# Kernel optimization log

Hardware: AMD Instinct MI355X
Metric: run time of the kernel (lower is better)

Reference implementation:

```python
import jax, jax.numpy as jnp
import numpy as np

N, E, G, H = 50000, 400000, 64, 128
NODE_IN, EDGE_IN = 3, 3
LN_EPS = 1e-5


def _ln(x, g, b):
    mu = jnp.mean(x, axis=-1, keepdims=True)
    var = jnp.mean((x - mu) ** 2, axis=-1, keepdims=True)
    return (x - mu) / jnp.sqrt(var + LN_EPS) * g + b


def _enc(x, w1, b1, w2, b2, w3, b3, g, bb):
    # Linear->ReLU->Linear->ReLU->Linear->LayerNorm (dropout = identity at eval)
    h = jax.nn.relu(x @ w1 + b1)
    h = jax.nn.relu(h @ w2 + b2)
    return _ln(h @ w3 + b3, g, bb)


def _gcn(x, w, b, src, dst, n):
    xw = x @ w
    deg = jax.ops.segment_sum(jnp.ones(src.shape[0], x.dtype), dst, num_segments=n) + 1.0
    dinv = jax.lax.rsqrt(deg)
    msgs = xw[src] * (dinv[src] * dinv[dst])[:, None]
    agg = jax.ops.segment_sum(msgs, dst, num_segments=n) + xw * (dinv * dinv)[:, None]
    return agg + b


def setup_inputs() -> dict:
    keys = iter(jax.random.split(jax.random.key(0), 64))

    def nrm(shape, s=0.05):
        return jax.random.normal(next(keys), shape, jnp.float32) * s

    inp = {
        "x": jax.random.normal(next(keys), (N, NODE_IN), jnp.float32),
        "edge_index": jax.random.randint(next(keys), (2, E), 0, N),
        "edge_attr": jax.random.normal(next(keys), (E, EDGE_IN), jnp.float32),
        "batch": jnp.sort(jax.random.randint(next(keys), (N,), 0, G)),
    }

    def lin(prefix, din, dout):
        inp[prefix + "_w"] = nrm((din, dout))
        inp[prefix + "_b"] = jnp.zeros((dout,), jnp.float32)

    for p, din in (("ne", NODE_IN), ("ee", EDGE_IN)):
        lin(p + "1", din, H); lin(p + "2", H, H); lin(p + "3", H, H)
        inp[p + "_g"] = jnp.ones((H,), jnp.float32)
        inp[p + "_bb"] = jnp.zeros((H,), jnp.float32)
    lin("g1", H, H); lin("g2", H, H)
    lin("gp1", H, H); lin("gp2", H, H)
    inp["gp_g"] = jnp.ones((H,), jnp.float32)
    inp["gp_bb"] = jnp.zeros((H,), jnp.float32)
    lin("ep1", 4 * H, 2 * H); lin("ep2", 2 * H, H)
    lin("ep3", H, H // 2); lin("ep4", H // 2, 1)
    return inp


def reference(x, edge_index, edge_attr, batch,
              ne1_w, ne1_b, ne2_w, ne2_b, ne3_w, ne3_b, ne_g, ne_bb,
              ee1_w, ee1_b, ee2_w, ee2_b, ee3_w, ee3_b, ee_g, ee_bb,
              g1_w, g1_b, g2_w, g2_b,
              gp1_w, gp1_b, gp2_w, gp2_b, gp_g, gp_bb,
              ep1_w, ep1_b, ep2_w, ep2_b, ep3_w, ep3_b, ep4_w, ep4_b):
    src, dst = edge_index[0], edge_index[1]
    h = _enc(x, ne1_w, ne1_b, ne2_w, ne2_b, ne3_w, ne3_b, ne_g, ne_bb)       # [N,H]
    ef = _enc(edge_attr, ee1_w, ee1_b, ee2_w, ee2_b, ee3_w, ee3_b, ee_g, ee_bb)  # [E,H]
    h = jax.nn.relu(_gcn(h, g1_w, g1_b, src, dst, N))
    h = _gcn(h, g2_w, g2_b, src, dst, N)
    # global mean pool per graph
    sums = jax.ops.segment_sum(h, batch, num_segments=G)
    cnts = jax.ops.segment_sum(jnp.ones((N,), h.dtype), batch, num_segments=G)
    gmean = sums / jnp.maximum(cnts, 1.0)[:, None]
    gf = jax.nn.relu(gmean @ gp1_w + gp1_b)
    gf = _ln(gf @ gp2_w + gp2_b, gp_g, gp_bb)                                 # [G,H]
    # vectorized edge-score MLP (original does a per-edge Python loop)
    comb = jnp.concatenate([h[src], h[dst], gf[batch[src]], ef], axis=-1)     # [E,4H]
    e = jnp.tanh(comb @ ep1_w + ep1_b)
    e = jnp.tanh(e @ ep2_w + ep2_b)
    e = jax.nn.relu(e @ ep3_w + ep3_b)
    return jax.nn.sigmoid(e @ ep4_w + ep4_b)                                  # [E,1]
```

## Files before the change

### kernel.cpp

```cpp
#include <hip/hip_runtime.h>
#include <math.h>

#define NN 50000
#define NE 400000
#define NG 64
#define HD 128
#define LN_EPS 1e-5f

typedef unsigned short u16;
typedef unsigned int u32;
typedef __attribute__((ext_vector_type(8))) short short8;
typedef __attribute__((ext_vector_type(4))) float f32x4;

#define MFMA16(a,b,c) __builtin_amdgcn_mfma_f32_16x16x32_bf16((a),(b),(c),0,0,0)

__device__ __forceinline__ u16 f2bf(float f) {
    union { float f; u32 u; } v; v.f = f;
    u32 r = v.u + 0x7FFFu + ((v.u >> 16) & 1u);
    return (u16)(r >> 16);
}
__device__ __forceinline__ float bf2f(u32 hs) {
    union { u32 u; float f; } v; v.u = hs << 16;
    return v.f;
}
__device__ __forceinline__ float fast_rcp(float x) {
    float r; asm("v_rcp_f32 %0, %1" : "=v"(r) : "v"(x)); return r;
}
__device__ __forceinline__ float fast_exp2(float x) {
    float r; asm("v_exp_f32 %0, %1" : "=v"(r) : "v"(x)); return r;
}
__device__ __forceinline__ u32 cvtpk(float lo, float hi) {
    u32 r; asm("v_cvt_pk_bf16_f32 %0, %1, %2" : "=v"(r) : "v"(lo), "v"(hi)); return r;
}
__device__ __forceinline__ float fast_tanh(float x) {
    return fmaf(-2.f, fast_rcp(1.f + fast_exp2(2.885390082f * x)), 1.f);
}
__device__ __forceinline__ float fast_sigmoid(float x) {
    return fast_rcp(1.f + fast_exp2(-1.442695041f * x));
}

__device__ __forceinline__ int swzr(int row) {
    return (row & 7) ^ ((row & 8) >> 2);
}

__device__ __forceinline__ short8 loadA(const u16* buf, int mi, int kk, int l) {
    int row = mi*16 + (l & 15);
    int ci  = (kk*4 + (l >> 4)) ^ swzr(l & 15);
    return *(const short8*)(buf + row*128 + (ci << 3));
}
__device__ __forceinline__ short8 loadB(const u16* wp, int nt, int ks, int nk, int l) {
    return *(const short8*)(wp + (((nt*nk + ks)*64 + l) << 3));
}

__device__ __forceinline__ void storeQuad(u32* buf, int R, int c, int l,
                                          float v0, float v1, float v2, float v3)
{
    int cw = c >> 1;
    int par = l & 1;
    float send = par ? v0 : v1;
    float recv = __shfl_xor(send, 1);
    int row = R + par;
    u32 word = par ? cvtpk(recv, v1) : cvtpk(v0, recv);
    buf[row*64 + (((cw >> 2) ^ swzr(row & 15)) << 2) + (cw & 3)] = word;
    send = par ? v2 : v3;
    recv = __shfl_xor(send, 1);
    row = R + 2 + par;
    word = par ? cvtpk(recv, v3) : cvtpk(v2, recv);
    buf[row*64 + (((cw >> 2) ^ swzr(row & 15)) << 2) + (cw & 3)] = word;
}

__device__ __forceinline__ void copyChunkOut(const u32* chunk, u32* gout, int n0, int t)
{
    for (int it = 0; it < 16; ++it) {
        int dw = it*256 + t;
        int row = dw >> 6, cw = dw & 63;
        if (n0 + row < NN)
            gout[(size_t)(n0 + row)*64 + cw] =
                chunk[row*64 + (((cw >> 2) ^ swzr(row & 15)) << 2) + (cw & 3)];
    }
}

__global__ __launch_bounds__(256)
void pack_all(const float* __restrict__ ee2w, const float* __restrict__ ee3w,
              const float* __restrict__ p1w,  const float* __restrict__ p2w,
              const float* __restrict__ p3w,  const float* __restrict__ ne2w,
              const float* __restrict__ ne3w, const float* __restrict__ g1w,
              const float* __restrict__ g2w,  u16* __restrict__ wpk)
{
    int idx = blockIdx.x*256 + threadIdx.x;
    if (idx >= 270336) return;
    const float* w; int K, N, local;
    if      (idx < 16384)  { w = ee2w; K = 128; N = 128; local = idx; }
    else if (idx < 32768)  { w = ee3w; K = 128; N = 128; local = idx - 16384; }
    else if (idx < 163840) { w = p1w;  K = 512; N = 256; local = idx - 32768; }
    else if (idx < 196608) { w = p2w;  K = 256; N = 128; local = idx - 163840; }
    else if (idx < 204800) { w = p3w;  K = 128; N = 64;  local = idx - 196608; }
    else if (idx < 221184) { w = ne2w; K = 128; N = 128; local = idx - 204800; }
    else if (idx < 237568) { w = ne3w; K = 128; N = 128; local = idx - 221184; }
    else if (idx < 253952) { w = g1w;  K = 128; N = 128; local = idx - 237568; }
    else                   { w = g2w;  K = 128; N = 128; local = idx - 253952; }
    int e = local & 7, l = (local >> 3) & 63, r = local >> 9;
    int nk = K >> 5;
    int nt = r / nk, kk = r % nk;
    int k = kk*32 + ((l >> 4) << 3) + e;
    int n = nt*16 + (l & 15);
    wpk[idx] = f2bf(w[k*N + n]);
}

__global__ __launch_bounds__(256)
void deg_count_int(const int* __restrict__ ei, int* __restrict__ degi)
{
    int e = blockIdx.x*256 + threadIdx.x;
    if (e < NE) atomicAdd(&degi[ei[NE + e]], 1);
}

__global__ __launch_bounds__(1024)
void scan_excl(const int* __restrict__ cnt, int* __restrict__ rp,
               float* __restrict__ dinv)
{
    __shared__ int wsum[16];
    __shared__ int carry;
    int t = threadIdx.x, lane = t & 63, w = t >> 6;
    int base = 0;
    for (int off = 0; off < NN; off += 4096) {
        int i0 = off + t*4;
        int v0 = (i0   < NN) ? cnt[i0]   : 0;
        int v1 = (i0+1 < NN) ? cnt[i0+1] : 0;
        int v2 = (i0+2 < NN) ? cnt[i0+2] : 0;
        int v3 = (i0+3 < NN) ? cnt[i0+3] : 0;
        int tot = v0 + v1 + v2 + v3;
        int s = tot;
#pragma unroll
        for (int d = 1; d < 64; d <<= 1) { int u = __shfl_up(s, d); if (lane >= d) s += u; }
        if (lane == 63) wsum[w] = s;
        __syncthreads();
        if (w == 0) {
            int wv = (lane < 16) ? wsum[lane] : 0;
            int ss = wv;
#pragma unroll
            for (int d = 1; d < 16; d <<= 1) { int u = __shfl_up(ss, d); if (lane >= d) ss += u; }
            if (lane < 16) wsum[lane] = ss - wv;
            if (lane == 15) carry = ss;
        }
        __syncthreads();
        int excl = base + wsum[w] + s - tot;
        if (i0   < NN) { rp[i0]   = excl;              dinv[i0]   = rsqrtf((float)v0 + 1.f); }
        if (i0+1 < NN) { rp[i0+1] = excl + v0;         dinv[i0+1] = rsqrtf((float)v1 + 1.f); }
        if (i0+2 < NN) { rp[i0+2] = excl + v0 + v1;    dinv[i0+2] = rsqrtf((float)v2 + 1.f); }
        if (i0+3 < NN) { rp[i0+3] = excl + v0 + v1 + v2; dinv[i0+3] = rsqrtf((float)v3 + 1.f); }
        base += carry;
        __syncthreads();
    }
    if (t == 0) rp[NN] = base;
}

__global__ __launch_bounds__(256)
void fill_csr(const int* __restrict__ ei, const int* __restrict__ rp,
              int* __restrict__ cursor, int* __restrict__ sadj)
{
    int e = blockIdx.x*256 + threadIdx.x;
    if (e >= NE) return;
    int d = ei[NE + e];
    int slot = atomicAdd(&cursor[d], 1);
    sadj[rp[d] + slot] = ei[e];
}

__global__ __launch_bounds__(256, 4)
void enc_mfma(const float* __restrict__ x,
              const float* __restrict__ w1, const float* __restrict__ b1,
              const u16* __restrict__ w2p, const float* __restrict__ b2,
              const u16* __restrict__ w3p, const float* __restrict__ b3,
              const float* __restrict__ gg, const float* __restrict__ bb,
              const u16* __restrict__ g1p, const float* __restrict__ dinv,
              u32* __restrict__ xw1p)
{
    __shared__ u16 chunkA[64*HD];
    __shared__ u16 chunkB[64*HD];
    __shared__ float sX[192];
    __shared__ float sDi[64];
    __shared__ float rstat[128];

    const int t = threadIdx.x;
    const int l = t & 63;
    const int wid = t >> 6;
    const int n0 = blockIdx.x * 64;

    if (t < 192) sX[t] = (n0*3 + t < NN*3) ? x[n0*3 + t] : 0.f;
    if (t < 64)  sDi[t] = (n0 + t < NN) ? dinv[n0 + t] : 0.f;
    __syncthreads();

    for (int it = 0; it < 16; ++it) {
        int dw = it*256 + t;
        int e = dw >> 6, cd = dw & 63;
        int c0 = cd*2;
        float x0 = sX[e*3], x1 = sX[e*3+1], x2 = sX[e*3+2];
        float v0 = b1[c0]   + x0*w1[c0]   + x1*w1[HD+c0]   + x2*w1[2*HD+c0];
        float v1 = b1[c0+1] + x0*w1[c0+1] + x1*w1[HD+c0+1] + x2*w1[2*HD+c0+1];
        v0 = fmaxf(v0, 0.f); v1 = fmaxf(v1, 0.f);
        int ci = cd >> 2;
        ((u32*)chunkA)[e*64 + ((ci ^ swzr(e & 15)) << 2) + (cd & 3)] = cvtpk(v0, v1);
    }
    __syncthreads();

    {
        f32x4 acc[4][2];
#pragma unroll
        for (int ni = 0; ni < 2; ++ni) {
            float b = b2[(2*wid + ni)*16 + (l & 15)];
#pragma unroll
            for (int mi = 0; mi < 4; ++mi) acc[mi][ni] = (f32x4){b,b,b,b};
        }
#pragma unroll
        for (int kk = 0; kk < 4; ++kk) {
            short8 af[4];
#pragma unroll
            for (int mi = 0; mi < 4; ++mi) af[mi] = loadA(chunkA, mi, kk, l);
#pragma unroll
            for (int ni = 0; ni < 2; ++ni) {
                short8 bw = loadB(w2p, 2*wid + ni, kk, 4, l);
#pragma unroll
                for (int mi = 0; mi < 4; ++mi) acc[mi][ni] = MFMA16(af[mi], bw, acc[mi][ni]);
            }
        }
#pragma unroll
        for (int ni = 0; ni < 2; ++ni) {
            int col = (2*wid + ni)*16 + (l & 15);
#pragma unroll
            for (int mi = 0; mi < 4; ++mi) {
                int R = mi*16 + ((l >> 4) << 2);
                storeQuad((u32*)chunkB, R, col, l,
                          fmaxf(acc[mi][ni][0], 0.f), fmaxf(acc[mi][ni][1], 0.f),
                          fmaxf(acc[mi][ni][2], 0.f), fmaxf(acc[mi][ni][3], 0.f));
            }
        }
    }
    __syncthreads();

    {
        f32x4 acc[4][2];
#pragma unroll
        for (int ni = 0; ni < 2; ++ni) {
            float b = b3[(2*wid + ni)*16 + (l & 15)];
#pragma unroll
            for (int mi = 0; mi < 4; ++mi) acc[mi][ni] = (f32x4){b,b,b,b};
        }
#pragma unroll
        for (int kk = 0; kk < 4; ++kk) {
            short8 af[4];
#pragma unroll
            for (int mi = 0; mi < 4; ++mi) af[mi] = loadA(chunkB, mi, kk, l);
#pragma unroll
            for (int ni = 0; ni < 2; ++ni) {
                short8 bw = loadB(w3p, 2*wid + ni, kk, 4, l);
#pragma unroll
                for (int mi = 0; mi < 4; ++mi) acc[mi][ni] = MFMA16(af[mi], bw, acc[mi][ni]);
            }
        }
#pragma unroll
        for (int ni = 0; ni < 2; ++ni) {
            int col = (2*wid + ni)*16 + (l & 15);
#pragma unroll
            for (int mi = 0; mi < 4; ++mi) {
                int R = mi*16 + ((l >> 4) << 2);
                storeQuad((u32*)chunkA, R, col, l,
                          acc[mi][ni][0], acc[mi][ni][1], acc[mi][ni][2], acc[mi][ni][3]);
            }
        }
    }
    __syncthreads();

    {
        int e = wid*16 + (l >> 2);
        int q = l & 3;
        const u32* rowp = (const u32*)chunkA + e*64;
        float s = 0.f, sq = 0.f;
#pragma unroll
        for (int i = 0; i < 16; ++i) {
            u32 pk = rowp[q*16 + ((i + e) & 15)];
            float a = bf2f(pk & 0xffffu), b = bf2f(pk >> 16);
            s += a + b;
            sq = fmaf(a, a, fmaf(b, b, sq));
        }
        s  += __shfl_xor(s, 1);  sq += __shfl_xor(sq, 1);
        s  += __shfl_xor(s, 2);  sq += __shfl_xor(sq, 2);
        if (q == 0) {
            float mu = s * (1.f/HD);
            rstat[e] = mu;
            rstat[64 + e] = rsqrtf(sq*(1.f/HD) - mu*mu + LN_EPS);
        }
    }
    __syncthreads();

    for (int it = 0; it < 16; ++it) {
        int pd = it*256 + t;
        int row = pd >> 6, cwd = pd & 63;
        int ci = (cwd >> 2) ^ swzr(row & 15);
        int col = ci*8 + (cwd & 3)*2;
        u32 pk = ((u32*)chunkA)[pd];
        float mu = rstat[row], ri = rstat[64 + row];
        float v0 = (bf2f(pk & 0xffffu) - mu)*ri*gg[col]     + bb[col];
        float v1 = (bf2f(pk >> 16)     - mu)*ri*gg[col + 1] + bb[col + 1];
        ((u32*)chunkA)[pd] = cvtpk(v0, v1);
    }
    __syncthreads();

    {
        f32x4 acc[4][2];
#pragma unroll
        for (int mi = 0; mi < 4; ++mi)
#pragma unroll
            for (int ni = 0; ni < 2; ++ni) acc[mi][ni] = (f32x4){0.f,0.f,0.f,0.f};
#pragma unroll
        for (int kk = 0; kk < 4; ++kk) {
            short8 af[4];
#pragma unroll
            for (int mi = 0; mi < 4; ++mi) af[mi] = loadA(chunkA, mi, kk, l);
#pragma unroll
            for (int ni = 0; ni < 2; ++ni) {
                short8 bw = loadB(g1p, 2*wid + ni, kk, 4, l);
#pragma unroll
                for (int mi = 0; mi < 4; ++mi) acc[mi][ni] = MFMA16(af[mi], bw, acc[mi][ni]);
            }
        }
#pragma unroll
        for (int ni = 0; ni < 2; ++ni) {
            int col = (2*wid + ni)*16 + (l & 15);
#pragma unroll
            for (int mi = 0; mi < 4; ++mi) {
                int R = mi*16 + ((l >> 4) << 2);
                storeQuad((u32*)chunkB, R, col, l,
                          acc[mi][ni][0]*sDi[R], acc[mi][ni][1]*sDi[R+1],
                          acc[mi][ni][2]*sDi[R+2], acc[mi][ni][3]*sDi[R+3]);
            }
        }
    }
    __syncthreads();
    copyChunkOut((const u32*)chunkB, xw1p, n0, t);
}

__global__ __launch_bounds__(256, 4)
void gcn_agg1_mfma(const u16* __restrict__ xw1p, const int* __restrict__ rp,
                   const int* __restrict__ sadj, const float* __restrict__ dinv,
                   const float* __restrict__ g1b, const u16* __restrict__ g2p,
                   u32* __restrict__ xw2p)
{
    __shared__ u16 chunkA[64*HD];
    __shared__ u16 chunkB[64*HD];
    __shared__ float sDi[64];
    __shared__ float sB[HD];

    const int t = threadIdx.x;
    const int l = t & 63;
    const int wid = t >> 6;
    const int n0 = blockIdx.x * 64;

    if (t < 64)  sDi[t] = (n0 + t < NN) ? dinv[n0 + t] : 0.f;
    if (t < HD)  sB[t] = g1b[t];
    __syncthreads();

    {
        int s = t >> 2, part = t & 3, n = n0 + s;
        float acc[32];
#pragma unroll
        for (int j = 0; j < 32; ++j) acc[j] = 0.f;
        float di = 0.f;
        if (n < NN) {
            di = sDi[s];
            const short8* selfp = (const short8*)(xw1p + (size_t)n*HD + part*32);
#pragma unroll
            for (int w = 0; w < 4; ++w) {
                short8 v = selfp[w];
#pragma unroll
                for (int j = 0; j < 8; ++j) acc[w*8+j] += bf2f((u16)v[j]);
            }
            int k1 = rp[n+1];
            for (int k = rp[n]; k < k1; ++k) {
                const short8* rp8 = (const short8*)(xw1p + (size_t)sadj[k]*HD + part*32);
#pragma unroll
                for (int w = 0; w < 4; ++w) {
                    short8 v = rp8[w];
#pragma unroll
                    for (int j = 0; j < 8; ++j) acc[w*8+j] += bf2f((u16)v[j]);
                }
            }
        }
#pragma unroll
        for (int p = 0; p < 16; ++p) {
            float v0 = fmaxf(fmaf(acc[2*p],   di, sB[part*32 + 2*p]),   0.f);
            float v1 = fmaxf(fmaf(acc[2*p+1], di, sB[part*32 + 2*p+1]), 0.f);
            int cw = part*16 + p;
            ((u32*)chunkA)[s*64 + (((cw >> 2) ^ swzr(s & 15)) << 2) + (cw & 3)] = cvtpk(v0, v1);
        }
    }
    __syncthreads();

    {
        f32x4 acc[4][2];
#pragma unroll
        for (int mi = 0; mi < 4; ++mi)
#pragma unroll
            for (int ni = 0; ni < 2; ++ni) acc[mi][ni] = (f32x4){0.f,0.f,0.f,0.f};
#pragma unroll
        for (int kk = 0; kk < 4; ++kk) {
            short8 af[4];
#pragma unroll
            for (int mi = 0; mi < 4; ++mi) af[mi] = loadA(chunkA, mi, kk, l);
#pragma unroll
            for (int ni = 0; ni < 2; ++ni) {
                short8 bw = loadB(g2p, 2*wid + ni, kk, 4, l);
#pragma unroll
                for (int mi = 0; mi < 4; ++mi) acc[mi][ni] = MFMA16(af[mi], bw, acc[mi][ni]);
            }
        }
#pragma unroll
        for (int ni = 0; ni < 2; ++ni) {
            int col = (2*wid + ni)*16 + (l & 15);
#pragma unroll
            for (int mi = 0; mi < 4; ++mi) {
                int R = mi*16 + ((l >> 4) << 2);
                storeQuad((u32*)chunkB, R, col, l,
                          acc[mi][ni][0]*sDi[R], acc[mi][ni][1]*sDi[R+1],
                          acc[mi][ni][2]*sDi[R+2], acc[mi][ni][3]*sDi[R+3]);
            }
        }
    }
    __syncthreads();
    copyChunkOut((const u32*)chunkB, xw2p, n0, t);
}

__global__ __launch_bounds__(256)
void gcn_agg2_gather(const u16* __restrict__ xw2p, const int* __restrict__ rp,
                     const int* __restrict__ sadj, const float* __restrict__ dinv,
                     const float* __restrict__ g2b, u32* __restrict__ hbw)
{
    int t = threadIdx.x;
    int s = t >> 2, part = t & 3;
    int n = blockIdx.x * 64 + s;
    if (n >= NN) return;
    float acc[32];
#pragma unroll
    for (int j = 0; j < 32; ++j) acc[j] = 0.f;
    const short8* selfp = (const short8*)(xw2p + (size_t)n*HD + part*32);
#pragma unroll
    for (int w = 0; w < 4; ++w) {
        short8 v = selfp[w];
#pragma unroll
        for (int j = 0; j < 8; ++j) acc[w*8+j] += bf2f((u16)v[j]);
    }
    int k1 = rp[n+1];
    for (int k = rp[n]; k < k1; ++k) {
        const short8* rp8 = (const short8*)(xw2p + (size_t)sadj[k]*HD + part*32);
#pragma unroll
        for (int w = 0; w < 4; ++w) {
            short8 v = rp8[w];
#pragma unroll
            for (int j = 0; j < 8; ++j) acc[w*8+j] += bf2f((u16)v[j]);
        }
    }
    float di = dinv[n];
    u32* hb = hbw + (size_t)n*64 + part*16;
#pragma unroll
    for (int p = 0; p < 16; ++p) {
        float v0 = fmaf(acc[2*p],   di, g2b[part*32 + 2*p]);
        float v1 = fmaf(acc[2*p+1], di, g2b[part*32 + 2*p+1]);
        hb[p] = cvtpk(v0, v1);
    }
}

#define POOL_B 512
__global__ __launch_bounds__(128)
void pool_sorted(const u16* __restrict__ h, const int* __restrict__ batch,
                 float* __restrict__ sums, float* __restrict__ cnts)
{
    int b = blockIdx.x, j = threadIdx.x;
    int n0 = (int)(((long long)NN * b) / POOL_B);
    int n1 = (int)(((long long)NN * (b+1)) / POOL_B);
    int g = -1; float acc = 0.f, cl = 0.f;
    for (int n = n0; n < n1; ++n) {
        int bg = batch[n];
        if (bg != g) {
            if (g >= 0) {
                atomicAdd(&sums[g*HD + j], acc);
                if (j == 0) atomicAdd(&cnts[g], cl);
            }
            g = bg; acc = 0.f; cl = 0.f;
        }
        acc += bf2f(h[(size_t)n*HD + j]);
        cl += 1.f;
    }
    if (g >= 0) {
        atomicAdd(&sums[g*HD + j], acc);
        if (j == 0) atomicAdd(&cnts[g], cl);
    }
}

__global__ __launch_bounds__(128)
void graph_feat(const float* __restrict__ sums, const float* __restrict__ cnts,
                const float* __restrict__ w1, const float* __restrict__ b1,
                const float* __restrict__ w2, const float* __restrict__ b2,
                const float* __restrict__ gg, const float* __restrict__ bb,
                u16* __restrict__ gf16)
{
    int gi = blockIdx.x, j = threadIdx.x;
    __shared__ float s0[HD];
    __shared__ float s1[HD];
    __shared__ float part[4];
    __shared__ float stat[2];
    float cnt = fmaxf(cnts[gi], 1.f);
    s0[j] = sums[gi*HD + j] / cnt;
    __syncthreads();
    float a = b1[j];
    for (int i = 0; i < HD; ++i) a = fmaf(s0[i], w1[i*HD + j], a);
    s1[j] = fmaxf(a, 0.f);
    __syncthreads();
    a = b2[j];
    for (int i = 0; i < HD; ++i) a = fmaf(s1[i], w2[i*HD + j], a);
    float s = a, q = a*a;
    for (int o = 32; o > 0; o >>= 1) { s += __shfl_down(s, o); q += __shfl_down(q, o); }
    int wid = j >> 6, lane = j & 63;
    if (lane == 0) { part[wid] = s; part[2 + wid] = q; }
    __syncthreads();
    if (j == 0) {
        float S = part[0] + part[1], Q = part[2] + part[3];
        float mu = S * (1.f/HD);
        stat[0] = mu;
        stat[1] = Q * (1.f/HD) - mu*mu;
    }
    __syncthreads();
    float v = (a - stat[0]) * rsqrtf(stat[1] + LN_EPS) * gg[j] + bb[j];
    gf16[gi*HD + j] = f2bf(v);
}

__device__ __forceinline__ void stageRows(u16* dst, const u16* __restrict__ srcBase,
                                          const int* ridx, int t)
{
    int e = t >> 2, part = t & 3;
    const u16* src = srcBase + (size_t)ridx[e]*HD + part*32;
    u16* drow = dst + e*128;
    int re = swzr(e & 15);
#pragma unroll
    for (int w = 0; w < 4; ++w) {
        int ci = (part*4 + w) ^ re;
        *(short8*)(drow + (ci << 3)) = *(const short8*)(src + w*8);
    }
}

__global__ __launch_bounds__(256, 2)
void edge_mlp_mfma(const u16* __restrict__ hbf, const u16* __restrict__ gfbf,
                   const int* __restrict__ ei, const int* __restrict__ batch,
                   const float* __restrict__ ea,
                   const float* __restrict__ ew1, const float* __restrict__ eb1,
                   const u16* __restrict__ ew2p, const float* __restrict__ eb2,
                   const u16* __restrict__ ew3p, const float* __restrict__ eb3,
                   const float* __restrict__ egm, const float* __restrict__ ebb,
                   const u16* __restrict__ p1wp, const float* __restrict__ p1b,
                   const u16* __restrict__ p2wp, const float* __restrict__ p2b,
                   const u16* __restrict__ p3wp, const float* __restrict__ p3b,
                   const float* __restrict__ p4w, const float* __restrict__ p4b,
                   float* __restrict__ out)
{
    __shared__ u16 bufChunk[64*HD];
    __shared__ u16 bufWide[64*256];
    __shared__ float sEa[192];
    __shared__ int sGf[64];
    __shared__ float rstat[128];

    const int t = threadIdx.x;
    const int l = t & 63;
    const int wid = t >> 6;
    const int e0 = blockIdx.x * 64;

    const int eRow = t >> 2, part = t & 3;
    int srcN = ei[e0 + eRow];
    int dstN = ei[NE + e0 + eRow];
    if (part == 0) sGf[eRow] = batch[srcN];
    short8 rs[4], rd[4];
    {
        const short8* ps = (const short8*)(hbf + (size_t)srcN*HD + part*32);
        const short8* pd = (const short8*)(hbf + (size_t)dstN*HD + part*32);
#pragma unroll
        for (int w = 0; w < 4; ++w) { rs[w] = ps[w]; rd[w] = pd[w]; }
    }

    if (t < 192) sEa[t] = ea[e0*3 + t];
    __syncthreads();

    for (int it = 0; it < 16; ++it) {
        int dw = it*256 + t;
        int e = dw >> 6, cd = dw & 63;
        int c0 = cd*2;
        float x0 = sEa[e*3], x1 = sEa[e*3+1], x2 = sEa[e*3+2];
        float v0 = eb1[c0]   + x0*ew1[c0]   + x1*ew1[HD+c0]   + x2*ew1[2*HD+c0];
        float v1 = eb1[c0+1] + x0*ew1[c0+1] + x1*ew1[HD+c0+1] + x2*ew1[2*HD+c0+1];
        v0 = fmaxf(v0, 0.f); v1 = fmaxf(v1, 0.f);
        int ci = cd >> 2;
        ((u32*)bufChunk)[e*64 + ((ci ^ swzr(e & 15)) << 2) + (cd & 3)] = cvtpk(v0, v1);
    }
    __syncthreads();

    {
        f32x4 acc[4][2];
#pragma unroll
        for (int ni = 0; ni < 2; ++ni) {
            float b = eb2[(2*wid + ni)*16 + (l & 15)];
#pragma unroll
            for (int mi = 0; mi < 4; ++mi) acc[mi][ni] = (f32x4){b,b,b,b};
        }
#pragma unroll
        for (int kk = 0; kk < 4; ++kk) {
            short8 af[4];
#pragma unroll
            for (int mi = 0; mi < 4; ++mi) af[mi] = loadA(bufChunk, mi, kk, l);
#pragma unroll
            for (int ni = 0; ni < 2; ++ni) {
                short8 bw = loadB(ew2p, 2*wid + ni, kk, 4, l);
#pragma unroll
                for (int mi = 0; mi < 4; ++mi) acc[mi][ni] = MFMA16(af[mi], bw, acc[mi][ni]);
            }
        }
#pragma unroll
        for (int ni = 0; ni < 2; ++ni) {
            int col = (2*wid + ni)*16 + (l & 15);
#pragma unroll
            for (int mi = 0; mi < 4; ++mi) {
                int R = mi*16 + ((l >> 4) << 2);
                storeQuad((u32*)bufWide, R, col, l,
                          fmaxf(acc[mi][ni][0], 0.f), fmaxf(acc[mi][ni][1], 0.f),
                          fmaxf(acc[mi][ni][2], 0.f), fmaxf(acc[mi][ni][3], 0.f));
            }
        }
    }
    __syncthreads();

    {
        f32x4 acc[4][2];
#pragma unroll
        for (int ni = 0; ni < 2; ++ni) {
            float b = eb3[(2*wid + ni)*16 + (l & 15)];
#pragma unroll
            for (int mi = 0; mi < 4; ++mi) acc[mi][ni] = (f32x4){b,b,b,b};
        }
#pragma unroll
        for (int kk = 0; kk < 4; ++kk) {
            short8 af[4];
#pragma unroll
            for (int mi = 0; mi < 4; ++mi) af[mi] = loadA(bufWide, mi, kk, l);
#pragma unroll
            for (int ni = 0; ni < 2; ++ni) {
                short8 bw = loadB(ew3p, 2*wid + ni, kk, 4, l);
#pragma unroll
                for (int mi = 0; mi < 4; ++mi) acc[mi][ni] = MFMA16(af[mi], bw, acc[mi][ni]);
            }
        }
#pragma unroll
        for (int ni = 0; ni < 2; ++ni) {
            int col = (2*wid + ni)*16 + (l & 15);
#pragma unroll
            for (int mi = 0; mi < 4; ++mi) {
                int R = mi*16 + ((l >> 4) << 2);
                storeQuad((u32*)bufChunk, R, col, l,
                          acc[mi][ni][0], acc[mi][ni][1], acc[mi][ni][2], acc[mi][ni][3]);
            }
        }
    }
    __syncthreads();

    {
        u16* drow0 = bufWide + eRow*128;
        u16* drow1 = bufWide + 8192 + eRow*128;
        int re = swzr(eRow & 15);
#pragma unroll
        for (int w = 0; w < 4; ++w) {
            int ci = (part*4 + w) ^ re;
            *(short8*)(drow0 + (ci << 3)) = rs[w];
            *(short8*)(drow1 + (ci << 3)) = rd[w];
        }
    }

    {
        int e = wid*16 + (l >> 2);
        int q = l & 3;
        const u32* rowp = (const u32*)bufChunk + e*64;
        float s = 0.f, sq = 0.f;
#pragma unroll
        for (int i = 0; i < 16; ++i) {
            u32 pk = rowp[q*16 + ((i + e) & 15)];
            float a = bf2f(pk & 0xffffu), b = bf2f(pk >> 16);
            s += a + b;
            sq = fmaf(a, a, fmaf(b, b, sq));
        }
        s  += __shfl_xor(s, 1);  sq += __shfl_xor(sq, 1);
        s  += __shfl_xor(s, 2);  sq += __shfl_xor(sq, 2);
        if (q == 0) {
            float mu = s * (1.f/HD);
            rstat[e] = mu;
            rstat[64 + e] = rsqrtf(sq*(1.f/HD) - mu*mu + LN_EPS);
        }
    }
    __syncthreads();

    for (int it = 0; it < 16; ++it) {
        int pd = it*256 + t;
        int row = pd >> 6, cwd = pd & 63;
        int ci = (cwd >> 2) ^ swzr(row & 15);
        int col = ci*8 + (cwd & 3)*2;
        u32 pk = ((u32*)bufChunk)[pd];
        float mu = rstat[row], ri = rstat[64 + row];
        float v0 = (bf2f(pk & 0xffffu) - mu)*ri*egm[col]     + ebb[col];
        float v1 = (bf2f(pk >> 16)     - mu)*ri*egm[col + 1] + ebb[col + 1];
        ((u32*)bufChunk)[pd] = cvtpk(v0, v1);
    }
    __syncthreads();

    f32x4 acc1[4][4];
#pragma unroll
    for (int ni = 0; ni < 4; ++ni) {
        float b = p1b[(4*wid + ni)*16 + (l & 15)];
#pragma unroll
        for (int mi = 0; mi < 4; ++mi) acc1[mi][ni] = (f32x4){b,b,b,b};
    }
#pragma unroll
    for (int kk = 0; kk < 4; ++kk) {
        short8 af[4];
#pragma unroll
        for (int mi = 0; mi < 4; ++mi) af[mi] = loadA(bufChunk, mi, kk, l);
#pragma unroll
        for (int ni = 0; ni < 4; ++ni) {
            short8 bw = loadB(p1wp, 4*wid + ni, 12 + kk, 16, l);
#pragma unroll
            for (int mi = 0; mi < 4; ++mi) acc1[mi][ni] = MFMA16(af[mi], bw, acc1[mi][ni]);
        }
    }
#pragma unroll
    for (int kk = 0; kk < 4; ++kk) {
        short8 af[4];
#pragma unroll
        for (int mi = 0; mi < 4; ++mi) af[mi] = loadA(bufWide, mi, kk, l);
#pragma unroll
        for (int ni = 0; ni < 4; ++ni) {
            short8 bw = loadB(p1wp, 4*wid + ni, kk, 16, l);
#pragma unroll
            for (int mi = 0; mi < 4; ++mi) acc1[mi][ni] = MFMA16(af[mi], bw, acc1[mi][ni]);
        }
    }
#pragma unroll
    for (int kk = 0; kk < 4; ++kk) {
        short8 af[4];
#pragma unroll
        for (int mi = 0; mi < 4; ++mi) af[mi] = loadA(bufWide + 8192, mi, kk, l);
#pragma unroll
        for (int ni = 0; ni < 4; ++ni) {
            short8 bw = loadB(p1wp, 4*wid + ni, 4 + kk, 16, l);
#pragma unroll
            for (int mi = 0; mi < 4; ++mi) acc1[mi][ni] = MFMA16(af[mi], bw, acc1[mi][ni]);
        }
    }
    __syncthreads();

    stageRows(bufChunk, gfbf, sGf, t);
    __syncthreads();
#pragma unroll
    for (int kk = 0; kk < 4; ++kk) {
        short8 af[4];
#pragma unroll
        for (int mi = 0; mi < 4; ++mi) af[mi] = loadA(bufChunk, mi, kk, l);
#pragma unroll
        for (int ni = 0; ni < 4; ++ni) {
            short8 bw = loadB(p1wp, 4*wid + ni, 8 + kk, 16, l);
#pragma unroll
            for (int mi = 0; mi < 4; ++mi) acc1[mi][ni] = MFMA16(af[mi], bw, acc1[mi][ni]);
        }
    }
#pragma unroll
    for (int ni = 0; ni < 4; ++ni) {
        int col = (4*wid + ni)*16 + (l & 15);
        u32* dst = (u32*)bufWide + ((col >> 7) << 12);
        int cc = col & 127;
#pragma unroll
        for (int mi = 0; mi < 4; ++mi) {
            int R = mi*16 + ((l >> 4) << 2);
            storeQuad(dst, R, cc, l,
                      fast_tanh(acc1[mi][ni][0]), fast_tanh(acc1[mi][ni][1]),
                      fast_tanh(acc1[mi][ni][2]), fast_tanh(acc1[mi][ni][3]));
        }
    }
    __syncthreads();

    {
        f32x4 acc[4][2];
#pragma unroll
        for (int ni = 0; ni < 2; ++ni) {
            float b = p2b[(2*wid + ni)*16 + (l & 15)];
#pragma unroll
            for (int mi = 0; mi < 4; ++mi) acc[mi][ni] = (f32x4){b,b,b,b};
        }
        for (int kc = 0; kc < 2; ++kc) {
            const u16* abuf = bufWide + (kc << 13);
#pragma unroll
            for (int kk = 0; kk < 4; ++kk) {
                short8 af[4];
#pragma unroll
                for (int mi = 0; mi < 4; ++mi) af[mi] = loadA(abuf, mi, kk, l);
                int ks = kc*4 + kk;
#pragma unroll
                for (int ni = 0; ni < 2; ++ni) {
                    short8 bw = loadB(p2wp, 2*wid + ni, ks, 8, l);
#pragma unroll
                    for (int mi = 0; mi < 4; ++mi) acc[mi][ni] = MFMA16(af[mi], bw, acc[mi][ni]);
                }
            }
        }
#pragma unroll
        for (int ni = 0; ni < 2; ++ni) {
            int col = (2*wid + ni)*16 + (l & 15);
#pragma unroll
            for (int mi = 0; mi < 4; ++mi) {
                int R = mi*16 + ((l >> 4) << 2);
                storeQuad((u32*)bufChunk, R, col, l,
                          fast_tanh(acc[mi][ni][0]), fast_tanh(acc[mi][ni][1]),
                          fast_tanh(acc[mi][ni][2]), fast_tanh(acc[mi][ni][3]));
            }
        }
    }
    __syncthreads();

    {
        f32x4 acc[4];
        {
            float b = p3b[wid*16 + (l & 15)];
#pragma unroll
            for (int mi = 0; mi < 4; ++mi) acc[mi] = (f32x4){b,b,b,b};
        }
#pragma unroll
        for (int kk = 0; kk < 4; ++kk) {
            short8 af[4];
#pragma unroll
            for (int mi = 0; mi < 4; ++mi) af[mi] = loadA(bufChunk, mi, kk, l);
            short8 bw = loadB(p3wp, wid, kk, 4, l);
#pragma unroll
            for (int mi = 0; mi < 4; ++mi) acc[mi] = MFMA16(af[mi], bw, acc[mi]);
        }
        float* fb = (float*)bufWide;
        int col = wid*16 + (l & 15);
#pragma unroll
        for (int mi = 0; mi < 4; ++mi)
#pragma unroll
            for (int rr = 0; rr < 4; ++rr) {
                int row = mi*16 + ((l >> 4) << 2) + rr;
                fb[row*65 + col] = fmaxf(acc[mi][rr], 0.f);
            }
    }
    __syncthreads();

    {
        const float* fb = (const float*)bufWide;
        int e = wid*16 + (l >> 2), q = l & 3;
        float v = 0.f;
#pragma unroll
        for (int k = 0; k < 16; ++k) {
            int i = q*16 + k;
            v = fmaf(fb[e*65 + i], p4w[i], v);
        }
        v += __shfl_xor(v, 1);
        v += __shfl_xor(v, 2);
        if (q == 0) out[e0 + e] = fast_sigmoid(v + p4b[0]);
    }
}

extern "C" void kernel_launch(void* const* d_in, const int* in_sizes, int n_in,
                              void* d_out, int out_size, void* d_ws, size_t ws_size,
                              hipStream_t stream)
{
    const float* x     = (const float*)d_in[0];
    const int*   ei    = (const int*)  d_in[1];
    const float* ea    = (const float*)d_in[2];
    const int*   batch = (const int*)  d_in[3];
    const float* ne1w = (const float*)d_in[4];  const float* ne1b = (const float*)d_in[5];
    const float* ne2w = (const float*)d_in[6];  const float* ne2b = (const float*)d_in[7];
    const float* ne3w = (const float*)d_in[8];  const float* ne3b = (const float*)d_in[9];
    const float* neg  = (const float*)d_in[10]; const float* nebb = (const float*)d_in[11];
    const float* ee1w = (const float*)d_in[12]; const float* ee1b = (const float*)d_in[13];
    const float* ee2w = (const float*)d_in[14]; const float* ee2b = (const float*)d_in[15];
    const float* ee3w = (const float*)d_in[16]; const float* ee3b = (const float*)d_in[17];
    const float* eeg  = (const float*)d_in[18]; const float* eebb = (const float*)d_in[19];
    const float* g1w  = (const float*)d_in[20]; const float* g1b  = (const float*)d_in[21];
    const float* g2w  = (const float*)d_in[22]; const float* g2b  = (const float*)d_in[23];
    const float* gp1w = (const float*)d_in[24]; const float* gp1b = (const float*)d_in[25];
    const float* gp2w = (const float*)d_in[26]; const float* gp2b = (const float*)d_in[27];
    const float* gpg  = (const float*)d_in[28]; const float* gpbb = (const float*)d_in[29];
    const float* p1w  = (const float*)d_in[30]; const float* p1b  = (const float*)d_in[31];
    const float* p2w  = (const float*)d_in[32]; const float* p2b  = (const float*)d_in[33];
    const float* p3w  = (const float*)d_in[34]; const float* p3b  = (const float*)d_in[35];
    const float* p4w  = (const float*)d_in[36]; const float* p4b  = (const float*)d_in[37];

    float* dinv = (float*)d_ws;
    float* sums = dinv + NN;
    float* cnts = sums + NG*HD;
    int* degi   = (int*)(cnts + NG);
    int* cursor = degi + NN;
    int* rowptr = cursor + NN + 2;
    int* sadj   = rowptr + NN + 2;
    u16* xw1p   = (u16*)(sadj + NE);
    u16* xw2p   = xw1p + (size_t)NN*HD;
    u16* hbf    = xw2p + (size_t)NN*HD;
    u16* gf16   = hbf + (size_t)NN*HD;
    u16* wpk    = gf16 + NG*HD;
    u16* ee2p = wpk;
    u16* ee3p = wpk + 16384;
    u16* p1p  = wpk + 32768;
    u16* p2p  = wpk + 163840;
    u16* p3p  = wpk + 196608;
    u16* ne2p = wpk + 204800;
    u16* ne3p = wpk + 221184;
    u16* g1p  = wpk + 237568;
    u16* g2p  = wpk + 253952;

    float* out = (float*)d_out;

    hipMemsetAsync(degi, 0, (size_t)(2*NN + 2)*sizeof(int), stream);
    hipMemsetAsync(sums, 0, (size_t)(NG*HD + NG)*sizeof(float), stream);

    pack_all<<<(270336 + 255)/256, 256, 0, stream>>>(ee2w, ee3w, p1w, p2w, p3w,
                                                     ne2w, ne3w, g1w, g2w, wpk);

    deg_count_int<<<(NE + 255)/256, 256, 0, stream>>>(ei, degi);
    scan_excl<<<1, 1024, 0, stream>>>(degi, rowptr, dinv);
    fill_csr<<<(NE + 255)/256, 256, 0, stream>>>(ei, rowptr, cursor, sadj);

    enc_mfma<<<(NN + 63)/64, 256, 0, stream>>>(x, ne1w, ne1b, ne2p, ne2b, ne3p, ne3b,
                                               neg, nebb, g1p, dinv, (u32*)xw1p);
    gcn_agg1_mfma<<<(NN + 63)/64, 256, 0, stream>>>(xw1p, rowptr, sadj, dinv,
                                                    g1b, g2p, (u32*)xw2p);
    gcn_agg2_gather<<<(NN + 63)/64, 256, 0, stream>>>(xw2p, rowptr, sadj, dinv,
                                                      g2b, (u32*)hbf);

    pool_sorted<<<POOL_B, 128, 0, stream>>>(hbf, batch, sums, cnts);
    graph_feat<<<NG, 128, 0, stream>>>(sums, cnts, gp1w, gp1b, gp2w, gp2b,
                                       gpg, gpbb, gf16);

    edge_mlp_mfma<<<NE/64, 256, 0, stream>>>(hbf, gf16, ei, batch, ea,
                                             ee1w, ee1b, ee2p, ee2b, ee3p, ee3b,
                                             eeg, eebb,
                                             p1p, p1b, p2p, p2b, p3p, p3b,
                                             p4w, p4b, out);
}
```

Measured before the change: 524.6 us.

## Double edge-MLP block to 512 threads, splitting N-tiles across eight waves

The edge MLP kernel now runs with 512 threads (8 waves) per 64-edge block instead of 256. Each wave owns half as many output column tiles in every MFMA GEMM stage, and the gather, encoder and LayerNorm loops are re-split for the wider block. The aim is more waves in flight to hide gather and LDS latency and to cut per-wave accumulator registers. In exchange, each wave reloads the same A fragments from LDS, an extra barrier is added, and half the waves recompute the redundant final 64-wide stage.

```diff
diff --git a/kernel.cpp b/kernel.cpp
--- a/kernel.cpp
+++ b/kernel.cpp
@@ -545,7 +545,7 @@
     }
 }
 
-__global__ __launch_bounds__(256, 2)
+__global__ __launch_bounds__(512, 3)
 void edge_mlp_mfma(const u16* __restrict__ hbf, const u16* __restrict__ gfbf,
                    const int* __restrict__ ei, const int* __restrict__ batch,
                    const float* __restrict__ ea,
@@ -570,23 +570,23 @@
     const int wid = t >> 6;
     const int e0 = blockIdx.x * 64;
 
-    const int eRow = t >> 2, part = t & 3;
+    const int eRow = t >> 3, part8 = t & 7;
     int srcN = ei[e0 + eRow];
     int dstN = ei[NE + e0 + eRow];
-    if (part == 0) sGf[eRow] = batch[srcN];
-    short8 rs[4], rd[4];
-    {
-        const short8* ps = (const short8*)(hbf + (size_t)srcN*HD + part*32);
-        const short8* pd = (const short8*)(hbf + (size_t)dstN*HD + part*32);
-#pragma unroll
-        for (int w = 0; w < 4; ++w) { rs[w] = ps[w]; rd[w] = pd[w]; }
+    if (part8 == 0) sGf[eRow] = batch[srcN];
+    short8 rs[2], rd[2];
+    {
+        const short8* ps = (const short8*)(hbf + (size_t)srcN*HD + part8*16);
+        const short8* pd = (const short8*)(hbf + (size_t)dstN*HD + part8*16);
+#pragma unroll
+        for (int w = 0; w < 2; ++w) { rs[w] = ps[w]; rd[w] = pd[w]; }
     }
 
     if (t < 192) sEa[t] = ea[e0*3 + t];
     __syncthreads();
 
-    for (int it = 0; it < 16; ++it) {
-        int dw = it*256 + t;
+    for (int it = 0; it < 8; ++it) {
+        int dw = it*512 + t;
         int e = dw >> 6, cd = dw & 63;
         int c0 = cd*2;
         float x0 = sEa[e*3], x1 = sEa[e*3+1], x2 = sEa[e*3+2];
@@ -599,68 +599,54 @@
     __syncthreads();
 
     {
-        f32x4 acc[4][2];
-#pragma unroll
-        for (int ni = 0; ni < 2; ++ni) {
-            float b = eb2[(2*wid + ni)*16 + (l & 15)];
-#pragma unroll
-            for (int mi = 0; mi < 4; ++mi) acc[mi][ni] = (f32x4){b,b,b,b};
+        f32x4 acc[4];
+        {
+            float b = eb2[wid*16 + (l & 15)];
+#pragma unroll
+            for (int mi = 0; mi < 4; ++mi) acc[mi] = (f32x4){b,b,b,b};
         }
 #pragma unroll
         for (int kk = 0; kk < 4; ++kk) {
             short8 af[4];
 #pragma unroll
             for (int mi = 0; mi < 4; ++mi) af[mi] = loadA(bufChunk, mi, kk, l);
-#pragma unroll
-            for (int ni = 0; ni < 2; ++ni) {
-                short8 bw = loadB(ew2p, 2*wid + ni, kk, 4, l);
-#pragma unroll
-                for (int mi = 0; mi < 4; ++mi) acc[mi][ni] = MFMA16(af[mi], bw, acc[mi][ni]);
-            }
-        }
-#pragma unroll
-        for (int ni = 0; ni < 2; ++ni) {
-            int col = (2*wid + ni)*16 + (l & 15);
-#pragma unroll
-            for (int mi = 0; mi < 4; ++mi) {
-                int R = mi*16 + ((l >> 4) << 2);
-                storeQuad((u32*)bufWide, R, col, l,
-                          fmaxf(acc[mi][ni][0], 0.f), fmaxf(acc[mi][ni][1], 0.f),
-                          fmaxf(acc[mi][ni][2], 0.f), fmaxf(acc[mi][ni][3], 0.f));
-            }
-        }
-    }
-    __syncthreads();
-
-    {
-        f32x4 acc[4][2];
-#pragma unroll
-        for (int ni = 0; ni < 2; ++ni) {
-            float b = eb3[(2*wid + ni)*16 + (l & 15)];
-#pragma unroll
-            for (int mi = 0; mi < 4; ++mi) acc[mi][ni] = (f32x4){b,b,b,b};
+            short8 bw = loadB(ew2p, wid, kk, 4, l);
+#pragma unroll
+            for (int mi = 0; mi < 4; ++mi) acc[mi] = MFMA16(af[mi], bw, acc[mi]);
+        }
+        int col = wid*16 + (l & 15);
+#pragma unroll
+        for (int mi = 0; mi < 4; ++mi) {
+            int R = mi*16 + ((l >> 4) << 2);
+            storeQuad((u32*)bufWide, R, col, l,
+                      fmaxf(acc[mi][0], 0.f), fmaxf(acc[mi][1], 0.f),
+                      fmaxf(acc[mi][2], 0.f), fmaxf(acc[mi][3], 0.f));
+        }
+    }
+    __syncthreads();
+
+    {
+        f32x4 acc[4];
+        {
+            float b = eb3[wid*16 + (l & 15)];
+#pragma unroll
+            for (int mi = 0; mi < 4; ++mi) acc[mi] = (f32x4){b,b,b,b};
         }
 #pragma unroll
         for (int kk = 0; kk < 4; ++kk) {
             short8 af[4];
 #pragma unroll
             for (int mi = 0; mi < 4; ++mi) af[mi] = loadA(bufWide, mi, kk, l);
-#pragma unroll
-            for (int ni = 0; ni < 2; ++ni) {
-                short8 bw = loadB(ew3p, 2*wid + ni, kk, 4, l);
-#pragma unroll
-                for (int mi = 0; mi < 4; ++mi) acc[mi][ni] = MFMA16(af[mi], bw, acc[mi][ni]);
-            }
-        }
-#pragma unroll
-        for (int ni = 0; ni < 2; ++ni) {
-            int col = (2*wid + ni)*16 + (l & 15);
-#pragma unroll
-            for (int mi = 0; mi < 4; ++mi) {
-                int R = mi*16 + ((l >> 4) << 2);
-                storeQuad((u32*)bufChunk, R, col, l,
-                          acc[mi][ni][0], acc[mi][ni][1], acc[mi][ni][2], acc[mi][ni][3]);
-            }
+            short8 bw = loadB(ew3p, wid, kk, 4, l);
+#pragma unroll
+            for (int mi = 0; mi < 4; ++mi) acc[mi] = MFMA16(af[mi], bw, acc[mi]);
+        }
+        int col = wid*16 + (l & 15);
+#pragma unroll
+        for (int mi = 0; mi < 4; ++mi) {
+            int R = mi*16 + ((l >> 4) << 2);
+            storeQuad((u32*)bufChunk, R, col, l,
+                      acc[mi][0], acc[mi][1], acc[mi][2], acc[mi][3]);
         }
     }
     __syncthreads();
@@ -670,27 +656,28 @@
         u16* drow1 = bufWide + 8192 + eRow*128;
         int re = swzr(eRow & 15);
 #pragma unroll
-        for (int w = 0; w < 4; ++w) {
-            int ci = (part*4 + w) ^ re;
+        for (int w = 0; w < 2; ++w) {
+            int ci = (part8*2 + w) ^ re;
             *(short8*)(drow0 + (ci << 3)) = rs[w];
             *(short8*)(drow1 + (ci << 3)) = rd[w];
         }
     }
 
     {
-        int e = wid*16 + (l >> 2);
-        int q = l & 3;
+        int e = wid*8 + (l >> 3);
+        int q = l & 7;
         const u32* rowp = (const u32*)bufChunk + e*64;
         float s = 0.f, sq = 0.f;
 #pragma unroll
-        for (int i = 0; i < 16; ++i) {
-            u32 pk = rowp[q*16 + ((i + e) & 15)];
+        for (int i = 0; i < 8; ++i) {
+            u32 pk = rowp[q*8 + ((i + e) & 7)];
             float a = bf2f(pk & 0xffffu), b = bf2f(pk >> 16);
             s += a + b;
             sq = fmaf(a, a, fmaf(b, b, sq));
         }
         s  += __shfl_xor(s, 1);  sq += __shfl_xor(sq, 1);
         s  += __shfl_xor(s, 2);  sq += __shfl_xor(sq, 2);
+        s  += __shfl_xor(s, 4);  sq += __shfl_xor(sq, 4);
         if (q == 0) {
             float mu = s * (1.f/HD);
             rstat[e] = mu;
@@ -699,8 +686,8 @@
     }
     __syncthreads();
 
-    for (int it = 0; it < 16; ++it) {
-        int pd = it*256 + t;
+    for (int it = 0; it < 8; ++it) {
+        int pd = it*512 + t;
         int row = pd >> 6, cwd = pd & 63;
         int ci = (cwd >> 2) ^ swzr(row & 15);
         int col = ci*8 + (cwd & 3)*2;
@@ -712,10 +699,10 @@
     }
     __syncthreads();
 
-    f32x4 acc1[4][4];
-#pragma unroll
-    for (int ni = 0; ni < 4; ++ni) {
-        float b = p1b[(4*wid + ni)*16 + (l & 15)];
+    f32x4 acc1[4][2];
+#pragma unroll
+    for (int ni = 0; ni < 2; ++ni) {
+        float b = p1b[(wid*2 + ni)*16 + (l & 15)];
 #pragma unroll
         for (int mi = 0; mi < 4; ++mi) acc1[mi][ni] = (f32x4){b,b,b,b};
     }
@@ -725,8 +712,8 @@
 #pragma unroll
         for (int mi = 0; mi < 4; ++mi) af[mi] = loadA(bufChunk, mi, kk, l);
 #pragma unroll
-        for (int ni = 0; ni < 4; ++ni) {
-            short8 bw = loadB(p1wp, 4*wid + ni, 12 + kk, 16, l);
+        for (int ni = 0; ni < 2; ++ni) {
+            short8 bw = loadB(p1wp, wid*2 + ni, 12 + kk, 16, l);
 #pragma unroll
             for (int mi = 0; mi < 4; ++mi) acc1[mi][ni] = MFMA16(af[mi], bw, acc1[mi][ni]);
         }
@@ -737,8 +724,8 @@
 #pragma unroll
         for (int mi = 0; mi < 4; ++mi) af[mi] = loadA(bufWide, mi, kk, l);
 #pragma unroll
-        for (int ni = 0; ni < 4; ++ni) {
-            short8 bw = loadB(p1wp, 4*wid + ni, kk, 16, l);
+        for (int ni = 0; ni < 2; ++ni) {
+            short8 bw = loadB(p1wp, wid*2 + ni, kk, 16, l);
 #pragma unroll
             for (int mi = 0; mi < 4; ++mi) acc1[mi][ni] = MFMA16(af[mi], bw, acc1[mi][ni]);
         }
@@ -749,15 +736,15 @@
 #pragma unroll
         for (int mi = 0; mi < 4; ++mi) af[mi] = loadA(bufWide + 8192, mi, kk, l);
 #pragma unroll
-        for (int ni = 0; ni < 4; ++ni) {
-            short8 bw = loadB(p1wp, 4*wid + ni, 4 + kk, 16, l);
+        for (int ni = 0; ni < 2; ++ni) {
+            short8 bw = loadB(p1wp, wid*2 + ni, 4 + kk, 16, l);
 #pragma unroll
             for (int mi = 0; mi < 4; ++mi) acc1[mi][ni] = MFMA16(af[mi], bw, acc1[mi][ni]);
         }
     }
     __syncthreads();
 
-    stageRows(bufChunk, gfbf, sGf, t);
+    if (t < 256) stageRows(bufChunk, gfbf, sGf, t);
     __syncthreads();
 #pragma unroll
     for (int kk = 0; kk < 4; ++kk) {
@@ -765,15 +752,16 @@
 #pragma unroll
         for (int mi = 0; mi < 4; ++mi) af[mi] = loadA(bufChunk, mi, kk, l);
 #pragma unroll
-        for (int ni = 0; ni < 4; ++ni) {
-            short8 bw = loadB(p1wp, 4*wid + ni, 8 + kk, 16, l);
+        for (int ni = 0; ni < 2; ++ni) {
+            short8 bw = loadB(p1wp, wid*2 + ni, 8 + kk, 16, l);
 #pragma unroll
             for (int mi = 0; mi < 4; ++mi) acc1[mi][ni] = MFMA16(af[mi], bw, acc1[mi][ni]);
         }
     }
-#pragma unroll
-    for (int ni = 0; ni < 4; ++ni) {
-        int col = (4*wid + ni)*16 + (l & 15);
+    __syncthreads();
+#pragma unroll
+    for (int ni = 0; ni < 2; ++ni) {
+        int col = (wid*2 + ni)*16 + (l & 15);
         u32* dst = (u32*)bufWide + ((col >> 7) << 12);
         int cc = col & 127;
 #pragma unroll
@@ -787,12 +775,11 @@
     __syncthreads();
 
     {
-        f32x4 acc[4][2];
-#pragma unroll
-        for (int ni = 0; ni < 2; ++ni) {
-            float b = p2b[(2*wid + ni)*16 + (l & 15)];
-#pragma unroll
-            for (int mi = 0; mi < 4; ++mi) acc[mi][ni] = (f32x4){b,b,b,b};
+        f32x4 acc[4];
+        {
+            float b = p2b[wid*16 + (l & 15)];
+#pragma unroll
+            for (int mi = 0; mi < 4; ++mi) acc[mi] = (f32x4){b,b,b,b};
         }
         for (int kc = 0; kc < 2; ++kc) {
             const u16* abuf = bufWide + (kc << 13);
@@ -801,33 +788,27 @@
                 short8 af[4];
 #pragma unroll
                 for (int mi = 0; mi < 4; ++mi) af[mi] = loadA(abuf, mi, kk, l);
-                int ks = kc*4 + kk;
-#pragma unroll
-                for (int ni = 0; ni < 2; ++ni) {
-                    short8 bw = loadB(p2wp, 2*wid + ni, ks, 8, l);
-#pragma unroll
-                    for (int mi = 0; mi < 4; ++mi) acc[mi][ni] = MFMA16(af[mi], bw, acc[mi][ni]);
-                }
-            }
-        }
-#pragma unroll
-        for (int ni = 0; ni < 2; ++ni) {
-            int col = (2*wid + ni)*16 + (l & 15);
-#pragma unroll
-            for (int mi = 0; mi < 4; ++mi) {
-                int R = mi*16 + ((l >> 4) << 2);
-                storeQuad((u32*)bufChunk, R, col, l,
-                          fast_tanh(acc[mi][ni][0]), fast_tanh(acc[mi][ni][1]),
-                          fast_tanh(acc[mi][ni][2]), fast_tanh(acc[mi][ni][3]));
-            }
-        }
-    }
-    __syncthreads();
-
-    {
+                short8 bw = loadB(p2wp, wid, kc*4 + kk, 8, l);
+#pragma unroll
+                for (int mi = 0; mi < 4; ++mi) acc[mi] = MFMA16(af[mi], bw, acc[mi]);
+            }
+        }
+        int col = wid*16 + (l & 15);
+#pragma unroll
+        for (int mi = 0; mi < 4; ++mi) {
+            int R = mi*16 + ((l >> 4) << 2);
+            storeQuad((u32*)bufChunk, R, col, l,
+                      fast_tanh(acc[mi][0]), fast_tanh(acc[mi][1]),
+                      fast_tanh(acc[mi][2]), fast_tanh(acc[mi][3]));
+        }
+    }
+    __syncthreads();
+
+    {
+        int wt = wid & 3;
         f32x4 acc[4];
         {
-            float b = p3b[wid*16 + (l & 15)];
+            float b = p3b[wt*16 + (l & 15)];
 #pragma unroll
             for (int mi = 0; mi < 4; ++mi) acc[mi] = (f32x4){b,b,b,b};
         }
@@ -836,25 +817,27 @@
             short8 af[4];
 #pragma unroll
             for (int mi = 0; mi < 4; ++mi) af[mi] = loadA(bufChunk, mi, kk, l);
-            short8 bw = loadB(p3wp, wid, kk, 4, l);
+            short8 bw = loadB(p3wp, wt, kk, 4, l);
 #pragma unroll
             for (int mi = 0; mi < 4; ++mi) acc[mi] = MFMA16(af[mi], bw, acc[mi]);
         }
-        float* fb = (float*)bufWide;
-        int col = wid*16 + (l & 15);
-#pragma unroll
-        for (int mi = 0; mi < 4; ++mi)
-#pragma unroll
-            for (int rr = 0; rr < 4; ++rr) {
-                int row = mi*16 + ((l >> 4) << 2) + rr;
-                fb[row*65 + col] = fmaxf(acc[mi][rr], 0.f);
-            }
+        if (wid < 4) {
+            float* fb = (float*)bufWide;
+            int col = wt*16 + (l & 15);
+#pragma unroll
+            for (int mi = 0; mi < 4; ++mi)
+#pragma unroll
+                for (int rr = 0; rr < 4; ++rr) {
+                    int row = mi*16 + ((l >> 4) << 2) + rr;
+                    fb[row*65 + col] = fmaxf(acc[mi][rr], 0.f);
+                }
+        }
     }
     __syncthreads();
 
     {
         const float* fb = (const float*)bufWide;
-        int e = wid*16 + (l >> 2), q = l & 3;
+        int e = (wid & 3)*16 + (l >> 2), q = l & 3;
         float v = 0.f;
 #pragma unroll
         for (int k = 0; k < 16; ++k) {
@@ -863,7 +846,7 @@
         }
         v += __shfl_xor(v, 1);
         v += __shfl_xor(v, 2);
-        if (q == 0) out[e0 + e] = fast_sigmoid(v + p4b[0]);
+        if (q == 0 && wid < 4) out[e0 + e] = fast_sigmoid(v + p4b[0]);
     }
 }
 
@@ -938,7 +921,7 @@
     graph_feat<<<NG, 128, 0, stream>>>(sums, cnts, gp1w, gp1b, gp2w, gp2b,
                                        gpg, gpbb, gf16);
 
-    edge_mlp_mfma<<<NE/64, 256, 0, stream>>>(hbf, gf16, ei, batch, ea,
+    edge_mlp_mfma<<<NE/64, 512, 0, stream>>>(hbf, gf16, ei, batch, ea,
                                              ee1w, ee1b, ee2p, ee2b, ee3p, ee3b,
                                              eeg, eebb,
                                              p1p, p1b, p2p, p2b, p3p, p3b,
```

Measured after the change: 451.5 us. 1.16x faster.
